# Performance work log

Hardware: AMD Instinct MI355X
Metric: run time of the kernel (lower is better)

Reference implementation:

```python
import jax, jax.numpy as jnp
import numpy as np

N = 100000          # num_nodes
OUT = 64            # out_channels
E = 3200000         # num edges (avg degree 32)


def setup_inputs() -> dict:
    key = jax.random.key(0)
    k1, k2, k3 = jax.random.split(key, 3)
    edge_index = jax.random.randint(k1, (2, E), 0, N, dtype=jnp.int64)
    # nn.Linear(num_nodes, out_channels): W is [out, in] = [OUT, N]
    bound = 1.0 / np.sqrt(N)
    W = jax.random.uniform(k2, (OUT, N), jnp.float32, -bound, bound)
    b = jax.random.uniform(k3, (OUT,), jnp.float32, -bound, bound)
    return {"edge_index": edge_index, "W": W, "b": b}


def reference(edge_index, W, b):
    # LINK forward: A = sparse COO adjacency (N x N, value 1 per edge,
    # duplicates accumulate), logits = A @ W.T + b.
    # Row i of A @ W.T = sum over edges (i -> j) of W[:, j].
    row, col = edge_index[0], edge_index[1]
    msgs = W.T[col]                                  # [E, OUT] gather of W columns
    logits = jax.ops.segment_sum(msgs, row, num_segments=N)  # [N, OUT]
    return logits + b
```

## Files before the change

### kernel.cpp

```cpp
#include <hip/hip_runtime.h>
#include <hip/hip_bf16.h>


#define OUTC 64
#define NFX  2048
#define SLAB 2560
#define EPB  12544
#define PT   1024

__device__ inline unsigned f2bf(float x) {
    unsigned u = __float_as_uint(x);
    return (u + 0x7FFFu + ((u >> 16) & 1u)) >> 16;
}
__device__ inline float bf_lo(unsigned u) { return __uint_as_float(u << 16); }
__device__ inline float bf_hi(unsigned u) { return __uint_as_float(u & 0xFFFF0000u); }

__global__ __launch_bounds__(PT) void part_trans(const int* __restrict__ rows,
                                                 const int* __restrict__ cols,
                                                 const float* __restrict__ W,
                                                 unsigned* __restrict__ WTh,
                                                 int* __restrict__ gcur,
                                                 unsigned* __restrict__ packed,
                                                 int E, int N, int NF) {
    __shared__ union {
        float tile[64][65];
        struct {
            unsigned lbuf[EPB];
            int cnt[NFX];
            int loff[NFX + 1];
            int lcur[NFX];
            int gbase[NFX];
            int partial[PT];
        } p1;
    } sh;
    const int tid = threadIdx.x;

    const int ntiles = (N + 63) >> 6;
    for (int t = blockIdx.x; t < ntiles; t += gridDim.x) {
        const int n0 = t * 64;
        {
            int o = tid >> 4, q = tid & 15;
            int nn = n0 + q * 4;
            if (nn + 3 < N) {
                float4 v = *(const float4*)(W + (size_t)o * N + nn);
                sh.tile[o][q * 4 + 0] = v.x;
                sh.tile[o][q * 4 + 1] = v.y;
                sh.tile[o][q * 4 + 2] = v.z;
                sh.tile[o][q * 4 + 3] = v.w;
            } else {
                for (int j = 0; j < 4; ++j)
                    sh.tile[o][q * 4 + j] = (nn + j < N) ? W[(size_t)o * N + nn + j] : 0.f;
            }
        }
        __syncthreads();
        #pragma unroll
        for (int k2 = 0; k2 < 2; ++k2) {
            int idx = tid + k2 * PT;
            int nl = idx >> 5, u = idx & 31;
            int nn = n0 + nl;
            if (nn < N)
                WTh[(size_t)nn * 32 + u] =
                    f2bf(sh.tile[2 * u][nl]) | (f2bf(sh.tile[2 * u + 1][nl]) << 16);
        }
        __syncthreads();
    }

    const int nchunks = (E + EPB - 1) / EPB;
    for (int c = blockIdx.x; c < nchunks; c += gridDim.x) {
        const int base = c * EPB;
        const int lim  = min(E, base + EPB);
        const int nE   = lim - base;

        for (int i = tid; i < NFX; i += PT) sh.p1.cnt[i] = 0;
        __syncthreads();

        for (int e = base + tid * 4; e + 3 < lim; e += PT * 4) {
            int4 r = *(const int4*)(rows + e);
            atomicAdd(&sh.p1.cnt[r.x >> 6], 1);
            atomicAdd(&sh.p1.cnt[r.y >> 6], 1);
            atomicAdd(&sh.p1.cnt[r.z >> 6], 1);
            atomicAdd(&sh.p1.cnt[r.w >> 6], 1);
        }
        {
            int ts = base + (nE & ~3);
            for (int e = ts + tid; e < lim; e += PT)
                atomicAdd(&sh.p1.cnt[rows[e] >> 6], 1);
        }
        __syncthreads();

        int v0 = sh.p1.cnt[2 * tid], v1 = sh.p1.cnt[2 * tid + 1];
        int s  = v0 + v1;
        sh.p1.partial[tid] = s;
        __syncthreads();
        for (int off = 1; off < PT; off <<= 1) {
            int t = 0;
            if (tid >= off) t = sh.p1.partial[tid - off];
            __syncthreads();
            if (tid >= off) sh.p1.partial[tid] += t;
            __syncthreads();
        }
        int ex = sh.p1.partial[tid] - s;
        sh.p1.loff[2 * tid]     = ex;
        sh.p1.loff[2 * tid + 1] = ex + v0;
        sh.p1.lcur[2 * tid]     = ex;
        sh.p1.lcur[2 * tid + 1] = ex + v0;
        if (tid == PT - 1) sh.p1.loff[NFX] = sh.p1.partial[PT - 1];
        __syncthreads();

        for (int b = tid; b < NF; b += PT) {
            int cc = sh.p1.cnt[b];
            sh.p1.gbase[b] = b * SLAB + (cc ? atomicAdd(&gcur[b], cc) : 0);
        }
        __syncthreads();

        for (int e = base + tid * 4; e + 3 < lim; e += PT * 4) {
            int4 r  = *(const int4*)(rows + e);
            int4 cc = *(const int4*)(cols + e);
            int p0 = atomicAdd(&sh.p1.lcur[r.x >> 6], 1);
            int p1 = atomicAdd(&sh.p1.lcur[r.y >> 6], 1);
            int p2 = atomicAdd(&sh.p1.lcur[r.z >> 6], 1);
            int p3 = atomicAdd(&sh.p1.lcur[r.w >> 6], 1);
            sh.p1.lbuf[p0] = ((unsigned)(r.x & 63) << 17) | (unsigned)cc.x;
            sh.p1.lbuf[p1] = ((unsigned)(r.y & 63) << 17) | (unsigned)cc.y;
            sh.p1.lbuf[p2] = ((unsigned)(r.z & 63) << 17) | (unsigned)cc.z;
            sh.p1.lbuf[p3] = ((unsigned)(r.w & 63) << 17) | (unsigned)cc.w;
        }
        {
            int ts = base + (nE & ~3);
            for (int e = ts + tid; e < lim; e += PT) {
                int r = rows[e];
                int p = atomicAdd(&sh.p1.lcur[r >> 6], 1);
                sh.p1.lbuf[p] = ((unsigned)(r & 63) << 17) | (unsigned)cols[e];
            }
        }
        __syncthreads();

        const int chunk = (nE + PT - 1) / PT;
        int i0 = tid * chunk;
        int i1 = min(nE, i0 + chunk);
        if (i0 < i1) {
            int lo = 0, hi = NFX;
            while (hi - lo > 1) {
                int mid = (lo + hi) >> 1;
                if (sh.p1.loff[mid] <= i0) lo = mid; else hi = mid;
            }
            int b = lo;
            for (int i = i0; i < i1; ++i) {
                while (i >= sh.p1.loff[b + 1]) ++b;
                int pos = sh.p1.gbase[b] + (i - sh.p1.loff[b]);
                if (pos < (b + 1) * SLAB)
                    packed[pos] = sh.p1.lbuf[i];
            }
        }
        __syncthreads();
    }
}

__global__ __launch_bounds__(256) void sort_gather2(const unsigned* __restrict__ WTh,
                                                    const unsigned* __restrict__ packed,
                                                    const int* __restrict__ gcur,
                                                    const float* __restrict__ bias,
                                                    float* __restrict__ out, int N) {
    __shared__ unsigned scol[SLAB];
    __shared__ int cw[4 * 64];
    __shared__ int off0[64], tend[64];
    const int b    = blockIdx.x;
    const int tid  = threadIdx.x;
    const int lane = tid & 63;
    const int w    = tid >> 6;
    const int start = b * SLAB;
    int size = gcur[b];
    if (size > SLAB) size = SLAB;

    if (tid < 256) cw[tid] = 0;
    __syncthreads();
    for (int e = tid; e < size; e += 256)
        atomicAdd(&cw[w * 64 + (packed[start + e] >> 17)], 1);
    __syncthreads();
    if (tid < 64) {
        int c0 = cw[tid], c1 = cw[64 + tid], c2 = cw[128 + tid], c3 = cw[192 + tid];
        int v = c0 + c1 + c2 + c3;
        int inc = v;
        #pragma unroll
        for (int d = 1; d < 64; d <<= 1) {
            int t = __shfl_up(inc, d, 64);
            if (lane >= d) inc += t;
        }
        int ex = inc - v;
        off0[tid] = ex;
        tend[tid] = inc;
        cw[tid]       = ex;
        cw[64 + tid]  = ex + c0;
        cw[128 + tid] = ex + c0 + c1;
        cw[192 + tid] = ex + c0 + c1 + c2;
    }
    __syncthreads();
    for (int e = tid; e < size; e += 256) {
        unsigned u = packed[start + e];
        int p = atomicAdd(&cw[w * 64 + (u >> 17)], 1);
        scol[p] = u & 0x1FFFFu;
    }
    __syncthreads();

    const int g = lane >> 3;
    const int q = lane & 7;
    const float4 b0 = *(const float4*)(bias + q * 8);
    const float4 b1 = *(const float4*)(bias + q * 8 + 4);
    #pragma unroll
    for (int rb = 0; rb < 64; rb += 32) {
        const int r = rb + w * 8 + g;
        const int n = b * 64 + r;
        const int s = off0[r];
        const int t = tend[r];
        float a0 = 0.f, a1 = 0.f, a2 = 0.f, a3 = 0.f;
        float a4 = 0.f, a5 = 0.f, a6 = 0.f, a7 = 0.f;
        int e = s;
        while (__any(e < t)) {
            bool p0 = (e < t), p1 = (e + 1 < t);
            unsigned c0 = p0 ? scol[e] : 0u;
            unsigned c1 = p1 ? scol[e + 1] : 0u;
            if (p0) {
                uint4 u = *(const uint4*)(WTh + (size_t)c0 * 32 + q * 4);
                a0 += bf_lo(u.x); a1 += bf_hi(u.x);
                a2 += bf_lo(u.y); a3 += bf_hi(u.y);
                a4 += bf_lo(u.z); a5 += bf_hi(u.z);
                a6 += bf_lo(u.w); a7 += bf_hi(u.w);
            }
            if (p1) {
                uint4 u = *(const uint4*)(WTh + (size_t)c1 * 32 + q * 4);
                a0 += bf_lo(u.x); a1 += bf_hi(u.x);
                a2 += bf_lo(u.y); a3 += bf_hi(u.y);
                a4 += bf_lo(u.z); a5 += bf_hi(u.z);
                a6 += bf_lo(u.w); a7 += bf_hi(u.w);
            }
            e += 2;
        }
        if (n < N) {
            float4 o1, o2;
            o1.x = a0 + b0.x; o1.y = a1 + b0.y; o1.z = a2 + b0.z; o1.w = a3 + b0.w;
            o2.x = a4 + b1.x; o2.y = a5 + b1.y; o2.z = a6 + b1.z; o2.w = a7 + b1.w;
            *(float4*)(out + (size_t)n * 64 + q * 8)     = o1;
            *(float4*)(out + (size_t)n * 64 + q * 8 + 4) = o2;
        }
    }
}

extern "C" void kernel_launch(void* const* d_in, const int* in_sizes, int n_in,
                              void* d_out, int out_size, void* d_ws, size_t ws_size,
                              hipStream_t stream) {
    const int*   edges = (const int*)d_in[0];
    const float* W     = (const float*)d_in[1];
    const float* bias  = (const float*)d_in[2];
    float*       out   = (float*)d_out;

    const int E  = in_sizes[0] / 2;
    const int N  = in_sizes[1] / OUTC;
    const int NF = (N + 63) / 64;

    char* ws = (char*)d_ws;
    size_t off = 0;
    unsigned* WTh = (unsigned*)(ws + off); off += (size_t)N * 32 * sizeof(unsigned);
    off = (off + 255) & ~(size_t)255;
    int* gcur = (int*)(ws + off);          off += (size_t)NF * sizeof(int);
    off = (off + 255) & ~(size_t)255;
    unsigned* packed = (unsigned*)(ws + off); off += (size_t)NF * SLAB * sizeof(unsigned);
    (void)ws_size;

    const int* rows = edges;
    const int* cols = edges + E;

    hipMemsetAsync(gcur, 0, (size_t)NF * sizeof(int), stream);
    part_trans<<<256, PT, 0, stream>>>(rows, cols, W, WTh, gcur, packed, E, N, NF);
    sort_gather2<<<NF, 256, 0, stream>>>(WTh, packed, gcur, bias, out, N);
}
```

Before: 180.0 us.

## Widen gather block to 512 threads with 4-aligned rows and 4-edge unroll

```diff
diff --git a/kernel.cpp b/kernel.cpp
--- a/kernel.cpp
+++ b/kernel.cpp
@@ -5,8 +5,10 @@
 #define OUTC 64
 #define NFX  2048
 #define SLAB 2560
+#define SCOLN (SLAB + 256)
 #define EPB  12544
 #define PT   1024
+#define GT   512
 
 __device__ inline unsigned f2bf(float x) {
     unsigned u = __float_as_uint(x);
@@ -156,13 +158,13 @@
     }
 }
 
-__global__ __launch_bounds__(256) void sort_gather2(const unsigned* __restrict__ WTh,
-                                                    const unsigned* __restrict__ packed,
-                                                    const int* __restrict__ gcur,
-                                                    const float* __restrict__ bias,
-                                                    float* __restrict__ out, int N) {
-    __shared__ unsigned scol[SLAB];
-    __shared__ int cw[4 * 64];
+__global__ __launch_bounds__(GT) void sort_gather3(const unsigned* __restrict__ WTh,
+                                                   const unsigned* __restrict__ packed,
+                                                   const int* __restrict__ gcur,
+                                                   const float* __restrict__ bias,
+                                                   float* __restrict__ out, int N) {
+    __shared__ __align__(16) unsigned scol[SCOLN];
+    __shared__ int cw[8 * 64];
     __shared__ int off0[64], tend[64];
     const int b    = blockIdx.x;
     const int tid  = threadIdx.x;
@@ -172,76 +174,101 @@
     int size = gcur[b];
     if (size > SLAB) size = SLAB;
 
-    if (tid < 256) cw[tid] = 0;
+    cw[tid] = 0;
+    for (int i = tid; i < SCOLN; i += GT) scol[i] = 0u;
     __syncthreads();
-    for (int e = tid; e < size; e += 256)
+
+    for (int e = tid; e < size; e += GT)
         atomicAdd(&cw[w * 64 + (packed[start + e] >> 17)], 1);
     __syncthreads();
+
     if (tid < 64) {
-        int c0 = cw[tid], c1 = cw[64 + tid], c2 = cw[128 + tid], c3 = cw[192 + tid];
-        int v = c0 + c1 + c2 + c3;
-        int inc = v;
+        int c0 = cw[tid],        c1 = cw[64 + tid],  c2 = cw[128 + tid], c3 = cw[192 + tid];
+        int c4 = cw[256 + tid],  c5 = cw[320 + tid], c6 = cw[384 + tid], c7 = cw[448 + tid];
+        int v  = c0 + c1 + c2 + c3 + c4 + c5 + c6 + c7;
+        int va = (v + 3) & ~3;
+        int inc = va;
         #pragma unroll
         for (int d = 1; d < 64; d <<= 1) {
             int t = __shfl_up(inc, d, 64);
             if (lane >= d) inc += t;
         }
-        int ex = inc - v;
+        int ex = inc - va;
         off0[tid] = ex;
-        tend[tid] = inc;
-        cw[tid]       = ex;
-        cw[64 + tid]  = ex + c0;
-        cw[128 + tid] = ex + c0 + c1;
-        cw[192 + tid] = ex + c0 + c1 + c2;
+        tend[tid] = ex + v;
+        int run = ex;
+        cw[tid]       = run; run += c0;
+        cw[64 + tid]  = run; run += c1;
+        cw[128 + tid] = run; run += c2;
+        cw[192 + tid] = run; run += c3;
+        cw[256 + tid] = run; run += c4;
+        cw[320 + tid] = run; run += c5;
+        cw[384 + tid] = run; run += c6;
+        cw[448 + tid] = run;
     }
     __syncthreads();
-    for (int e = tid; e < size; e += 256) {
+
+    for (int e = tid; e < size; e += GT) {
         unsigned u = packed[start + e];
         int p = atomicAdd(&cw[w * 64 + (u >> 17)], 1);
         scol[p] = u & 0x1FFFFu;
     }
     __syncthreads();
 
-    const int g = lane >> 3;
-    const int q = lane & 7;
-    const float4 b0 = *(const float4*)(bias + q * 8);
-    const float4 b1 = *(const float4*)(bias + q * 8 + 4);
+    const int g = tid >> 3;
+    const int q = tid & 7;
+    const unsigned* Wq = WTh + q * 4;
+    const float4 bv0 = *(const float4*)(bias + q * 8);
+    const float4 bv1 = *(const float4*)(bias + q * 8 + 4);
+    const int s = off0[g];
+    const int t = tend[g];
+    float a0 = 0.f, a1 = 0.f, a2 = 0.f, a3 = 0.f;
+    float a4 = 0.f, a5 = 0.f, a6 = 0.f, a7 = 0.f;
+
+    int mx = t - s;
     #pragma unroll
-    for (int rb = 0; rb < 64; rb += 32) {
-        const int r = rb + w * 8 + g;
-        const int n = b * 64 + r;
-        const int s = off0[r];
-        const int t = tend[r];
-        float a0 = 0.f, a1 = 0.f, a2 = 0.f, a3 = 0.f;
-        float a4 = 0.f, a5 = 0.f, a6 = 0.f, a7 = 0.f;
-        int e = s;
-        while (__any(e < t)) {
-            bool p0 = (e < t), p1 = (e + 1 < t);
-            unsigned c0 = p0 ? scol[e] : 0u;
-            unsigned c1 = p1 ? scol[e + 1] : 0u;
-            if (p0) {
-                uint4 u = *(const uint4*)(WTh + (size_t)c0 * 32 + q * 4);
-                a0 += bf_lo(u.x); a1 += bf_hi(u.x);
-                a2 += bf_lo(u.y); a3 += bf_hi(u.y);
-                a4 += bf_lo(u.z); a5 += bf_hi(u.z);
-                a6 += bf_lo(u.w); a7 += bf_hi(u.w);
-            }
-            if (p1) {
-                uint4 u = *(const uint4*)(WTh + (size_t)c1 * 32 + q * 4);
-                a0 += bf_lo(u.x); a1 += bf_hi(u.x);
-                a2 += bf_lo(u.y); a3 += bf_hi(u.y);
-                a4 += bf_lo(u.z); a5 += bf_hi(u.z);
-                a6 += bf_lo(u.w); a7 += bf_hi(u.w);
-            }
-            e += 2;
-        }
-        if (n < N) {
-            float4 o1, o2;
-            o1.x = a0 + b0.x; o1.y = a1 + b0.y; o1.z = a2 + b0.z; o1.w = a3 + b0.w;
-            o2.x = a4 + b1.x; o2.y = a5 + b1.y; o2.z = a6 + b1.z; o2.w = a7 + b1.w;
-            *(float4*)(out + (size_t)n * 64 + q * 8)     = o1;
-            *(float4*)(out + (size_t)n * 64 + q * 8 + 4) = o2;
-        }
+    for (int d = 8; d < 64; d <<= 1) {
+        int o = __shfl_xor(mx, d, 64);
+        mx = mx > o ? mx : o;
+    }
+
+    int e = s;
+    for (int it = (mx + 3) >> 2; it > 0; --it, e += 4) {
+        if (e < t) {
+            uint4 cc = *(const uint4*)(scol + e);
+            uint4 u0 = *(const uint4*)(Wq + ((size_t)(cc.x << 5)));
+            uint4 u1 = *(const uint4*)(Wq + ((size_t)(cc.y << 5)));
+            uint4 u2 = *(const uint4*)(Wq + ((size_t)(cc.z << 5)));
+            uint4 u3 = *(const uint4*)(Wq + ((size_t)(cc.w << 5)));
+            float m1 = (e + 1 < t) ? 1.f : 0.f;
+            float m2 = (e + 2 < t) ? 1.f : 0.f;
+            float m3 = (e + 3 < t) ? 1.f : 0.f;
+            a0 += bf_lo(u0.x); a1 += bf_hi(u0.x);
+            a2 += bf_lo(u0.y); a3 += bf_hi(u0.y);
+            a4 += bf_lo(u0.z); a5 += bf_hi(u0.z);
+            a6 += bf_lo(u0.w); a7 += bf_hi(u0.w);
+            a0 = fmaf(m1, bf_lo(u1.x), a0); a1 = fmaf(m1, bf_hi(u1.x), a1);
+            a2 = fmaf(m1, bf_lo(u1.y), a2); a3 = fmaf(m1, bf_hi(u1.y), a3);
+            a4 = fmaf(m1, bf_lo(u1.z), a4); a5 = fmaf(m1, bf_hi(u1.z), a5);
+            a6 = fmaf(m1, bf_lo(u1.w), a6); a7 = fmaf(m1, bf_hi(u1.w), a7);
+            a0 = fmaf(m2, bf_lo(u2.x), a0); a1 = fmaf(m2, bf_hi(u2.x), a1);
+            a2 = fmaf(m2, bf_lo(u2.y), a2); a3 = fmaf(m2, bf_hi(u2.y), a3);
+            a4 = fmaf(m2, bf_lo(u2.z), a4); a5 = fmaf(m2, bf_hi(u2.z), a5);
+            a6 = fmaf(m2, bf_lo(u2.w), a6); a7 = fmaf(m2, bf_hi(u2.w), a7);
+            a0 = fmaf(m3, bf_lo(u3.x), a0); a1 = fmaf(m3, bf_hi(u3.x), a1);
+            a2 = fmaf(m3, bf_lo(u3.y), a2); a3 = fmaf(m3, bf_hi(u3.y), a3);
+            a4 = fmaf(m3, bf_lo(u3.z), a4); a5 = fmaf(m3, bf_hi(u3.z), a5);
+            a6 = fmaf(m3, bf_lo(u3.w), a6); a7 = fmaf(m3, bf_hi(u3.w), a7);
+        }
+    }
+
+    const int n = b * 64 + g;
+    if (n < N) {
+        float4 o1, o2;
+        o1.x = a0 + bv0.x; o1.y = a1 + bv0.y; o1.z = a2 + bv0.z; o1.w = a3 + bv0.w;
+        o2.x = a4 + bv1.x; o2.y = a5 + bv1.y; o2.z = a6 + bv1.z; o2.w = a7 + bv1.w;
+        *(float4*)(out + (size_t)n * 64 + q * 8)     = o1;
+        *(float4*)(out + (size_t)n * 64 + q * 8 + 4) = o2;
     }
 }
 
@@ -271,5 +298,5 @@
 
     hipMemsetAsync(gcur, 0, (size_t)NF * sizeof(int), stream);
     part_trans<<<256, PT, 0, stream>>>(rows, cols, W, WTh, gcur, packed, E, N, NF);
-    sort_gather2<<<NF, 256, 0, stream>>>(WTh, packed, gcur, bias, out, N);
+    sort_gather3<<<NF, GT, 0, stream>>>(WTh, packed, gcur, bias, out, N);
 }
```

Result: faster. 175.4 us (-2.6%).
